# Performance work log

Measured on AMD Instinct MI355X. Metric: run time of the kernel, lower is better.

The kernel has to match this reference:

```python
import jax, jax.numpy as jnp
import numpy as np

N = 50000   # nodes
E = 800000  # edges
IN, HID, HEADS, OUT = 128, 32, 4, 64
NEG_SLOPE = 0.2


def _gatv2_layer(x, src, dst, Wl, bl, Wr, br, att, bias, res_W, concat):
    """One PyG-style GATv2Conv layer (eval mode, no dropout).
    x: [N, F_in]; att: [H, C]. Returns [N, H*C] if concat else [N, C]."""
    H, C = att.shape
    xl = (x @ Wl + bl).reshape(N, H, C)   # source transform
    xr = (x @ Wr + br).reshape(N, H, C)   # target transform
    e = jax.nn.leaky_relu(xl[src] + xr[dst], NEG_SLOPE)        # [E, H, C]
    logit = jnp.einsum('ehc,hc->eh', e, att)                   # [E, H]
    # segment softmax over incoming edges per destination node
    m = jax.ops.segment_max(logit, dst, num_segments=N)        # [N, H]
    p = jnp.exp(logit - m[dst])
    denom = jax.ops.segment_sum(p, dst, num_segments=N)
    alpha = p / (denom[dst] + 1e-16)                           # [E, H]
    out = jax.ops.segment_sum(xl[src] * alpha[:, :, None], dst, num_segments=N)  # [N, H, C]
    out = out.reshape(N, H * C) if concat else out.mean(axis=1)
    if res_W is not None:
        out = out + x @ res_W
    return out + bias


def _glorot(key, shape):
    fan_in = shape[0] if len(shape) > 1 else shape[-1]
    return jax.random.normal(key, shape, dtype=jnp.float32) / np.sqrt(fan_in)


def setup_inputs() -> dict:
    key = jax.random.key(0)
    ks = iter(jax.random.split(key, 32))
    x = jax.random.normal(next(ks), (N, IN), dtype=jnp.float32)
    edge_index = jax.random.randint(next(ks), (2, E), 0, N, dtype=jnp.int64)
    d = {"x": x, "edge_index": edge_index}
    HC = HEADS * HID  # 128
    # layer 0: IN -> HEADS*HID, concat, residual
    d["Wl0"] = _glorot(next(ks), (IN, HC)); d["bl0"] = jnp.zeros((HC,), jnp.float32)
    d["Wr0"] = _glorot(next(ks), (IN, HC)); d["br0"] = jnp.zeros((HC,), jnp.float32)
    d["att0"] = _glorot(next(ks), (HEADS, HID)); d["b0"] = jnp.zeros((HC,), jnp.float32)
    d["res0"] = _glorot(next(ks), (IN, HC))
    # layer 1: HC -> HEADS*HID, concat, residual
    d["Wl1"] = _glorot(next(ks), (HC, HC)); d["bl1"] = jnp.zeros((HC,), jnp.float32)
    d["Wr1"] = _glorot(next(ks), (HC, HC)); d["br1"] = jnp.zeros((HC,), jnp.float32)
    d["att1"] = _glorot(next(ks), (HEADS, HID)); d["b1"] = jnp.zeros((HC,), jnp.float32)
    d["res1"] = _glorot(next(ks), (HC, HC))
    # layer 2: HC -> OUT, heads=1, concat=False, no residual
    d["Wl2"] = _glorot(next(ks), (HC, OUT)); d["bl2"] = jnp.zeros((OUT,), jnp.float32)
    d["Wr2"] = _glorot(next(ks), (HC, OUT)); d["br2"] = jnp.zeros((OUT,), jnp.float32)
    d["att2"] = _glorot(next(ks), (1, OUT)); d["b2"] = jnp.zeros((OUT,), jnp.float32)
    return d


def reference(x, edge_index,
              Wl0, bl0, Wr0, br0, att0, b0, res0,
              Wl1, bl1, Wr1, br1, att1, b1, res1,
              Wl2, bl2, Wr2, br2, att2, b2):
    src, dst = edge_index[0], edge_index[1]
    h = _gatv2_layer(x, src, dst, Wl0, bl0, Wr0, br0, att0, b0, res0, True)
    h = jax.nn.elu(h)
    h = _gatv2_layer(h, src, dst, Wl1, bl1, Wr1, br1, att1, b1, res1, True)
    h = jax.nn.elu(h)
    return _gatv2_layer(h, src, dst, Wl2, bl2, Wr2, br2, att2, b2, None, False)
```

## Files before the change

kernel.cpp:

```cpp
#include <hip/hip_runtime.h>
#include <math.h>

#define NN 50000
#define EE 800000
#define NBK 196
#define EPB 4096

typedef short v8s __attribute__((ext_vector_type(8)));
typedef float v4f __attribute__((ext_vector_type(4)));

__device__ __forceinline__ ushort f2bf(float f) {
    uint u = __float_as_uint(f);
    uint r = (u + 0x7fffu + ((u >> 16) & 1u)) >> 16;
    return (ushort)r;
}
__device__ __forceinline__ float bf2f(ushort h) {
    return __uint_as_float(((uint)h) << 16);
}
__device__ __forceinline__ float lrelu(float x) {
    return fmaf(0.4f, fabsf(x), 0.6f * x);
}

__device__ __forceinline__ void gld_lds16(const void* g, void* l) {
    __builtin_amdgcn_global_load_lds(
        (const __attribute__((address_space(1))) void*)g,
        (__attribute__((address_space(3))) void*)l, 16, 0, 0);
}

template <int CTRL>
__device__ __forceinline__ float dppadd(float x) {
    int y = __builtin_amdgcn_update_dpp(0, __float_as_int(x), CTRL, 0xf, 0xf, true);
    return x + __int_as_float(y);
}
__device__ __forceinline__ float sum8(float x) {
    x = dppadd<0xB1>(x);
    x = dppadd<0x4E>(x);
    x = dppadd<0x141>(x);
    return x;
}
__device__ __forceinline__ float sum16(float x) {
    x = sum8(x);
    x = dppadd<0x140>(x);
    return x;
}
__device__ __forceinline__ float expclamp(float t) {
    return __expf(fminf(fmaxf(t, -60.f), 80.f));
}

__global__ __launch_bounds__(256) void k_bktcnt(const int* __restrict__ edst,
                                                int* __restrict__ bcnt) {
    __shared__ int h[NBK];
    int t = threadIdx.x;
    if (t < NBK) h[t] = 0;
    __syncthreads();
    int eb = blockIdx.x * EPB;
    #pragma unroll
    for (int k = 0; k < EPB / 256; ++k) {
        int e = eb + k * 256 + t;
        if (e < EE) atomicAdd(&h[edst[e] >> 8], 1);
    }
    __syncthreads();
    if (t < NBK && h[t]) atomicAdd(&bcnt[t], h[t]);
}

__global__ __launch_bounds__(256) void k_bscan(const int* __restrict__ bcnt,
                                               int* __restrict__ bbase,
                                               int* __restrict__ bcur) {
    __shared__ int sm[256];
    int t = threadIdx.x;
    int v = (t < NBK) ? bcnt[t] : 0;
    sm[t] = v;
    __syncthreads();
    for (int o = 1; o < 256; o <<= 1) {
        int a = (t >= o) ? sm[t - o] : 0;
        __syncthreads();
        sm[t] += a;
        __syncthreads();
    }
    if (t < NBK) { int ex = sm[t] - v; bbase[t] = ex; bcur[t] = ex; }
}

__global__ __launch_bounds__(256) void k_bktplace(const int* __restrict__ esrc,
                                                  const int* __restrict__ edst,
                                                  int* __restrict__ bcur,
                                                  uint* __restrict__ ebuf) {
    __shared__ int h[NBK];
    __shared__ int base[NBK];
    int t = threadIdx.x;
    if (t < NBK) h[t] = 0;
    __syncthreads();
    int eb = blockIdx.x * EPB;
    int pk[EPB / 256];
    #pragma unroll
    for (int k = 0; k < EPB / 256; ++k) {
        int e = eb + k * 256 + t;
        pk[k] = -1;
        if (e < EE) {
            int b = edst[e] >> 8;
            int r = atomicAdd(&h[b], 1);
            pk[k] = (b << 16) | r;
        }
    }
    __syncthreads();
    if (t < NBK && h[t]) base[t] = atomicAdd(&bcur[t], h[t]);
    __syncthreads();
    #pragma unroll
    for (int k = 0; k < EPB / 256; ++k) {
        int e = eb + k * 256 + t;
        if (e < EE) {
            int b = pk[k] >> 16;
            int r = pk[k] & 0xFFFF;
            uint dl = (uint)(edst[e] & 255);
            ebuf[base[b] + r] = (dl << 16) | (uint)esrc[e];
        }
    }
}

__global__ __launch_bounds__(256) void k_bktfin(const uint* __restrict__ ebuf,
                                                const int* __restrict__ bbase,
                                                const int* __restrict__ bcnt,
                                                int* __restrict__ rowptr,
                                                int* __restrict__ csrc) {
    __shared__ int deg[256];
    __shared__ int sm[256];
    __shared__ int cur[256];
    const int b = blockIdx.x;
    const int t = threadIdx.x;
    const int eb = bbase[b];
    const int ec = bcnt[b];
    deg[t] = 0;
    __syncthreads();
    for (int k = t; k < ec; k += 256)
        atomicAdd(&deg[ebuf[eb + k] >> 16], 1);
    __syncthreads();
    int v = deg[t];
    sm[t] = v;
    __syncthreads();
    for (int o = 1; o < 256; o <<= 1) {
        int a = (t >= o) ? sm[t - o] : 0;
        __syncthreads();
        sm[t] += a;
        __syncthreads();
    }
    int node = b * 256 + t;
    if (node < NN) rowptr[node + 1] = eb + sm[t];
    if (node == 0) rowptr[0] = 0;
    cur[t] = sm[t] - v;
    __syncthreads();
    for (int k = t; k < ec; k += 256) {
        uint u = ebuf[eb + k];
        int nl = (int)(u >> 16);
        int r = atomicAdd(&cur[nl], 1);
        csrc[eb + r] = (int)(u & 0xFFFFu);
    }
}

struct WPack {
    const float* W[8];
    ushort* Th[8];
    ushort* Tl[8];
    int fout[8];
};

__global__ __launch_bounds__(256) void k_conv_w(WPack p) {
    int wi = blockIdx.y;
    int fout = p.fout[wi];
    int total = 128 * fout;
    int i = blockIdx.x * 256 + threadIdx.x;
    if (i >= total) return;
    int k = i / fout;
    int n = i - k * fout;
    float f = p.W[wi][i];
    ushort h = f2bf(f);
    float lo = f - bf2f(h);
    int t = n >> 4, m = n & 15, c = k >> 5, quad = (k >> 3) & 3, j = k & 7;
    int flat = ((((t * 4 + c) * 4 + quad) * 16 + m) << 3) + j;
    p.Th[wi][flat] = h;
    p.Tl[wi][flat] = f2bf(lo);
}

template <int FOUT, int NMAT, bool CVT, int TS>
__global__ __launch_bounds__(512) void k_gemm_fused(
    const float* __restrict__ Xf,
    const ushort* __restrict__ Xh, const ushort* __restrict__ Xl,
    const ushort* __restrict__ T0h, const ushort* __restrict__ T0l, const float* __restrict__ B0,
    const ushort* __restrict__ T1h, const ushort* __restrict__ T1l, const float* __restrict__ B1,
    const ushort* __restrict__ T2h, const ushort* __restrict__ T2l,
    const float* __restrict__ ATT, float* __restrict__ DL, float* __restrict__ DR,
    ushort* __restrict__ O0b, ushort* __restrict__ O1b, float* __restrict__ O2)
{
    constexpr int CH = TS * 2048;
    __shared__ __align__(16) ushort Bs[NMAT * 2 * CH];

    const int tid  = threadIdx.x;
    const int lane = tid & 63;
    const int wid  = tid >> 6;
    const int m    = lane & 15;
    const int quad = lane >> 4;
    const int row0 = blockIdx.x * 128 + wid * 16;
    const int t0   = blockIdx.y * TS;

    {
        const ushort* tbls[6] = {T0h, T0l, T1h, T1l, T2h, T2l};
        #pragma unroll
        for (int k = 0; k < 2 * NMAT; ++k) {
            gld_lds16(tbls[k] + (size_t)t0 * 2048 + (size_t)tid * 8,
                      &Bs[k * CH + tid * 8]);
        }
    }

    v8s ah[4], al[4];
    {
        int arow = row0 + m;
        if (arow > NN - 1) arow = NN - 1;
        #pragma unroll
        for (int c = 0; c < 4; ++c) {
            size_t off = (size_t)arow * 128 + c * 32 + quad * 8;
            if constexpr (CVT) {
                float4 f0 = *(const float4*)(Xf + off);
                float4 f1 = *(const float4*)(Xf + off + 4);
                const float fe[8] = {f0.x, f0.y, f0.z, f0.w, f1.x, f1.y, f1.z, f1.w};
                #pragma unroll
                for (int e = 0; e < 8; ++e) {
                    ushort h = f2bf(fe[e]);
                    float lo = fe[e] - bf2f(h);
                    ah[c][e] = (short)h;
                    al[c][e] = (short)(__float_as_uint(lo) >> 16);
                }
            } else {
                ah[c] = *(const v8s*)(Xh + off);
                al[c] = *(const v8s*)(Xl + off);
            }
        }
    }

    __syncthreads();

    float dp0[4] = {0.f, 0.f, 0.f, 0.f};
    float dp1[4] = {0.f, 0.f, 0.f, 0.f};

    #pragma unroll
    for (int tt = 0; tt < TS; ++tt) {
        const int t = t0 + tt;
        v4f a0 = {0.f, 0.f, 0.f, 0.f};
        v4f a1 = {0.f, 0.f, 0.f, 0.f};
        v4f a2 = {0.f, 0.f, 0.f, 0.f};
        #pragma unroll
        for (int c = 0; c < 4; ++c) {
            const int fo = tt * 2048 + (c * 4 + quad) * 128 + m * 8;
            v8s b0h = *(const v8s*)&Bs[0 * CH + fo];
            v8s b0l = *(const v8s*)&Bs[1 * CH + fo];
            v8s b1h = *(const v8s*)&Bs[2 * CH + fo];
            v8s b1l = *(const v8s*)&Bs[3 * CH + fo];
            a0 = __builtin_amdgcn_mfma_f32_16x16x32_bf16(al[c], b0h, a0, 0, 0, 0);
            a1 = __builtin_amdgcn_mfma_f32_16x16x32_bf16(al[c], b1h, a1, 0, 0, 0);
            a0 = __builtin_amdgcn_mfma_f32_16x16x32_bf16(ah[c], b0l, a0, 0, 0, 0);
            a1 = __builtin_amdgcn_mfma_f32_16x16x32_bf16(ah[c], b1l, a1, 0, 0, 0);
            a0 = __builtin_amdgcn_mfma_f32_16x16x32_bf16(ah[c], b0h, a0, 0, 0, 0);
            a1 = __builtin_amdgcn_mfma_f32_16x16x32_bf16(ah[c], b1h, a1, 0, 0, 0);
            if constexpr (NMAT == 3) {
                v8s b2h = *(const v8s*)&Bs[4 * CH + fo];
                v8s b2l = *(const v8s*)&Bs[5 * CH + fo];
                a2 = __builtin_amdgcn_mfma_f32_16x16x32_bf16(al[c], b2h, a2, 0, 0, 0);
                a2 = __builtin_amdgcn_mfma_f32_16x16x32_bf16(ah[c], b2l, a2, 0, 0, 0);
                a2 = __builtin_amdgcn_mfma_f32_16x16x32_bf16(ah[c], b2h, a2, 0, 0, 0);
            }
        }
        const int col = t * 16 + m;
        const float bad0 = B0[col];
        const float bad1 = B1[col];
        const float attc = ATT[col];
        #pragma unroll
        for (int j = 0; j < 4; ++j) {
            float o0v = a0[j] + bad0;
            float o1v = a1[j] + bad1;
            dp0[j] = fmaf(attc, o0v, dp0[j]);
            dp1[j] = fmaf(attc, o1v, dp1[j]);
            int r = row0 + quad * 4 + j;
            if (r < NN) {
                O0b[(size_t)r * FOUT + col] = f2bf(o0v);
                O1b[(size_t)r * FOUT + col] = f2bf(o1v);
                if constexpr (NMAT == 3) O2[(size_t)r * FOUT + col] = a2[j];
            }
        }
        if constexpr (FOUT == 128) {
            if ((t & 1) == 1) {
                const int h = t >> 1;
                #pragma unroll
                for (int j = 0; j < 4; ++j) {
                    float s0 = sum16(dp0[j]);
                    float s1 = sum16(dp1[j]);
                    int r = row0 + quad * 4 + j;
                    if (m == 0 && r < NN) {
                        DL[(size_t)r * 4 + h] = 0.6f * s0;
                        DR[(size_t)r * 4 + h] = 0.6f * s1;
                    }
                    dp0[j] = 0.f;
                    dp1[j] = 0.f;
                }
            }
        }
    }
    if constexpr (FOUT == 64) {
        #pragma unroll
        for (int j = 0; j < 4; ++j) {
            float s0 = sum16(dp0[j]);
            float s1 = sum16(dp1[j]);
            int r = row0 + quad * 4 + j;
            if (m == 0 && r < NN) {
                atomicAdd(&DL[r], 0.6f * s0);
                atomicAdd(&DR[r], 0.6f * s1);
            }
        }
    }
}

__global__ __launch_bounds__(256) void k_agg01(const ushort* __restrict__ XLb,
                                               const ushort* __restrict__ XRb,
                                               const float4* __restrict__ RES4,
                                               const float* __restrict__ att,
                                               const float* __restrict__ bias,
                                               const float* __restrict__ DL,
                                               const float* __restrict__ DR,
                                               const int* __restrict__ rowptr,
                                               const int* __restrict__ csrc,
                                               ushort* __restrict__ Hh,
                                               ushort* __restrict__ Hl) {
    const int lane = threadIdx.x & 63;
    const int wid = threadIdx.x >> 6;
    const int n = blockIdx.x * 4 + wid;
    if (n >= NN) return;
    const int beg = rowptr[n];
    const int end = rowptr[n + 1];
    const int e1 = end - 1;
    const int half = lane >> 5;
    const uint j = lane & 31;
    const uint head = j >> 3;

    float4 xr;
    {
        ushort4 u = *(const ushort4*)(XRb + (uint)n * 128u + 4u * j);
        xr.x = bf2f(u.x); xr.y = bf2f(u.y); xr.z = bf2f(u.z); xr.w = bf2f(u.w);
    }
    float4 at = ((const float4*)att)[j];
    at.x *= 0.4f; at.y *= 0.4f; at.z *= 0.4f; at.w *= 0.4f;
    const float dRn = DR[(uint)n * 4u + head];
    float4 s = {0.f, 0.f, 0.f, 0.f};
    float d = 0.f;

#define GL01(I, U0, U1, U2, U3, D0, D1, D2, D3) {              \
    uint sa = (uint)csrc[min((I) + half, e1)];                 \
    uint sb = (uint)csrc[min((I) + 2 + half, e1)];             \
    uint sc = (uint)csrc[min((I) + 4 + half, e1)];             \
    uint sd = (uint)csrc[min((I) + 6 + half, e1)];             \
    U0 = *(const ushort4*)(XLb + sa * 128u + 4u * j);          \
    U1 = *(const ushort4*)(XLb + sb * 128u + 4u * j);          \
    U2 = *(const ushort4*)(XLb + sc * 128u + 4u * j);          \
    U3 = *(const ushort4*)(XLb + sd * 128u + 4u * j);          \
    D0 = DL[sa * 4u + head];                                   \
    D1 = DL[sb * 4u + head];                                   \
    D2 = DL[sc * 4u + head];                                   \
    D3 = DL[sd * 4u + head]; }

#define EDGE01(U, DLV, II) {                                   \
    float v0 = bf2f((U).x), v1 = bf2f((U).y);                  \
    float v2 = bf2f((U).z), v3 = bf2f((U).w);                  \
    float t =      at.x * fabsf(v0 + xr.x);                    \
    t = fmaf(at.y, fabsf(v1 + xr.y), t);                       \
    t = fmaf(at.z, fabsf(v2 + xr.z), t);                       \
    t = fmaf(at.w, fabsf(v3 + xr.w), t);                       \
    float p = expclamp(sum8(t) + (DLV) + dRn);                 \
    p = ((II) < end) ? p : 0.f;                                \
    d += p;                                                    \
    s.x = fmaf(p, v0, s.x); s.y = fmaf(p, v1, s.y);            \
    s.z = fmaf(p, v2, s.z); s.w = fmaf(p, v3, s.w); }

    if (beg < end) {
        ushort4 cu0, cu1, cu2, cu3;
        float cd0, cd1, cd2, cd3;
        GL01(beg, cu0, cu1, cu2, cu3, cd0, cd1, cd2, cd3)
        for (int i = beg; i < end; i += 8) {
            ushort4 nu0, nu1, nu2, nu3;
            float nd0, nd1, nd2, nd3;
            GL01(i + 8, nu0, nu1, nu2, nu3, nd0, nd1, nd2, nd3)
            EDGE01(cu0, cd0, i + half)
            EDGE01(cu1, cd1, i + 2 + half)
            EDGE01(cu2, cd2, i + 4 + half)
            EDGE01(cu3, cd3, i + 6 + half)
            cu0 = nu0; cu1 = nu1; cu2 = nu2; cu3 = nu3;
            cd0 = nd0; cd1 = nd1; cd2 = nd2; cd3 = nd3;
        }
    }
#undef GL01
#undef EDGE01

    d   += __shfl_xor(d, 32);
    s.x += __shfl_xor(s.x, 32);
    s.y += __shfl_xor(s.y, 32);
    s.z += __shfl_xor(s.z, 32);
    s.w += __shfl_xor(s.w, 32);

    if (half == 0) {
        float inv = (d > 0.f) ? 1.f / d : 0.f;
        float4 rv = RES4[(uint)n * 32u + j];
        float4 bv = ((const float4*)bias)[j];
        float o0 = fmaf(s.x, inv, rv.x + bv.x);
        float o1 = fmaf(s.y, inv, rv.y + bv.y);
        float o2 = fmaf(s.z, inv, rv.z + bv.z);
        float o3 = fmaf(s.w, inv, rv.w + bv.w);
        o0 = o0 > 0.f ? o0 : __expf(o0) - 1.f;
        o1 = o1 > 0.f ? o1 : __expf(o1) - 1.f;
        o2 = o2 > 0.f ? o2 : __expf(o2) - 1.f;
        o3 = o3 > 0.f ? o3 : __expf(o3) - 1.f;
        ushort4 h, l;
        h.x = f2bf(o0); l.x = f2bf(o0 - bf2f(h.x));
        h.y = f2bf(o1); l.y = f2bf(o1 - bf2f(h.y));
        h.z = f2bf(o2); l.z = f2bf(o2 - bf2f(h.z));
        h.w = f2bf(o3); l.w = f2bf(o3 - bf2f(h.w));
        *(ushort4*)(Hh + (uint)n * 128u + 4u * j) = h;
        *(ushort4*)(Hl + (uint)n * 128u + 4u * j) = l;
    }
}

__global__ __launch_bounds__(256) void k_agg2(const ushort* __restrict__ XLb,
                                              const ushort* __restrict__ XRb,
                                              const float* __restrict__ att,
                                              const float* __restrict__ bias,
                                              const float* __restrict__ DL,
                                              const float* __restrict__ DR,
                                              const int* __restrict__ rowptr,
                                              const int* __restrict__ csrc,
                                              float* __restrict__ OUT) {
    const int lane = threadIdx.x & 63;
    const int wid = threadIdx.x >> 6;
    const int n = blockIdx.x * 4 + wid;
    if (n >= NN) return;
    const int beg = rowptr[n];
    const int end = rowptr[n + 1];
    const int e1 = end - 1;
    const int q = lane >> 4;
    const uint jj = lane & 15;

    float4 xr;
    {
        ushort4 u = *(const ushort4*)(XRb + (uint)n * 64u + 4u * jj);
        xr.x = bf2f(u.x); xr.y = bf2f(u.y); xr.z = bf2f(u.z); xr.w = bf2f(u.w);
    }
    float4 at = ((const float4*)att)[jj];
    at.x *= 0.4f; at.y *= 0.4f; at.z *= 0.4f; at.w *= 0.4f;
    const float dRn = DR[n];
    float4 s = {0.f, 0.f, 0.f, 0.f};
    float d = 0.f;

#define GL2(I, U0, U1, D0, D1) {                               \
    uint sa = (uint)csrc[min((I) + q, e1)];                    \
    uint sb = (uint)csrc[min((I) + 4 + q, e1)];                \
    U0 = *(const ushort4*)(XLb + sa * 64u + 4u * jj);          \
    U1 = *(const ushort4*)(XLb + sb * 64u + 4u * jj);          \
    D0 = DL[sa];                                               \
    D1 = DL[sb]; }

#define EDGE2(U, DLV, II) {                                    \
    float v0 = bf2f((U).x), v1 = bf2f((U).y);                  \
    float v2 = bf2f((U).z), v3 = bf2f((U).w);                  \
    float t =      at.x * fabsf(v0 + xr.x);                    \
    t = fmaf(at.y, fabsf(v1 + xr.y), t);                       \
    t = fmaf(at.z, fabsf(v2 + xr.z), t);                       \
    t = fmaf(at.w, fabsf(v3 + xr.w), t);                       \
    float p = expclamp(sum16(t) + (DLV) + dRn);                \
    p = ((II) < end) ? p : 0.f;                                \
    d += p;                                                    \
    s.x = fmaf(p, v0, s.x); s.y = fmaf(p, v1, s.y);            \
    s.z = fmaf(p, v2, s.z); s.w = fmaf(p, v3, s.w); }

    if (beg < end) {
        ushort4 cu0, cu1;
        float cd0, cd1;
        GL2(beg, cu0, cu1, cd0, cd1)
        for (int i = beg; i < end; i += 8) {
            ushort4 nu0, nu1;
            float nd0, nd1;
            GL2(i + 8, nu0, nu1, nd0, nd1)
            EDGE2(cu0, cd0, i + q)
            EDGE2(cu1, cd1, i + 4 + q)
            cu0 = nu0; cu1 = nu1;
            cd0 = nd0; cd1 = nd1;
        }
    }
#undef GL2
#undef EDGE2

    d   += __shfl_xor(d, 16);   d   += __shfl_xor(d, 32);
    s.x += __shfl_xor(s.x, 16); s.x += __shfl_xor(s.x, 32);
    s.y += __shfl_xor(s.y, 16); s.y += __shfl_xor(s.y, 32);
    s.z += __shfl_xor(s.z, 16); s.z += __shfl_xor(s.z, 32);
    s.w += __shfl_xor(s.w, 16); s.w += __shfl_xor(s.w, 32);

    if (lane < 16) {
        float inv = (d > 0.f) ? 1.f / d : 0.f;
        float4 bv = ((const float4*)bias)[jj];
        float4 o;
        o.x = fmaf(s.x, inv, bv.x);
        o.y = fmaf(s.y, inv, bv.y);
        o.z = fmaf(s.z, inv, bv.z);
        o.w = fmaf(s.w, inv, bv.w);
        *(float4*)(OUT + (uint)n * 64u + 4u * jj) = o;
    }
}

extern "C" void kernel_launch(void* const* d_in, const int* in_sizes, int n_in,
                              void* d_out, int out_size, void* d_ws, size_t ws_size,
                              hipStream_t stream) {
    const float* x    = (const float*)d_in[0];
    const int*   ei   = (const int*)d_in[1];
    const int*   esrc = ei;
    const int*   edst = ei + EE;

    const float* Wl0 = (const float*)d_in[2];
    const float* bl0 = (const float*)d_in[3];
    const float* Wr0 = (const float*)d_in[4];
    const float* br0 = (const float*)d_in[5];
    const float* at0 = (const float*)d_in[6];
    const float* b0  = (const float*)d_in[7];
    const float* rs0 = (const float*)d_in[8];
    const float* Wl1 = (const float*)d_in[9];
    const float* bl1 = (const float*)d_in[10];
    const float* Wr1 = (const float*)d_in[11];
    const float* br1 = (const float*)d_in[12];
    const float* at1 = (const float*)d_in[13];
    const float* b1  = (const float*)d_in[14];
    const float* rs1 = (const float*)d_in[15];
    const float* Wl2 = (const float*)d_in[16];
    const float* bl2 = (const float*)d_in[17];
    const float* Wr2 = (const float*)d_in[18];
    const float* br2 = (const float*)d_in[19];
    const float* at2 = (const float*)d_in[20];
    const float* b2  = (const float*)d_in[21];

    float* out = (float*)d_out;

    ushort* XLb = (ushort*)d_ws;
    ushort* XRb = XLb + (size_t)NN * 128;
    float* RES = (float*)(XRb + (size_t)NN * 128);
    ushort* Xh = (ushort*)(RES + (size_t)NN * 128);
    ushort* Xl_ = Xh + (size_t)NN * 128;
    float* DLarr = (float*)(Xl_ + (size_t)NN * 128);
    float* DRarr = DLarr + (size_t)NN * 4;
    ushort* Wth = (ushort*)(DRarr + (size_t)NN * 4);
    const int wsz[8] = {16384, 16384, 16384, 16384, 16384, 16384, 8192, 8192};
    ushort* th[8]; ushort* tl[8];
    {
        ushort* p = Wth;
        for (int i = 0; i < 8; ++i) { th[i] = p; p += wsz[i]; }
        for (int i = 0; i < 8; ++i) { tl[i] = p; p += wsz[i]; }
    }
    int* bcnt   = (int*)(Wth + 2 * (6 * 16384 + 2 * 8192));
    int* bbase  = bcnt + 256;
    int* bcur   = bbase + 256;
    int* rowptr = bcur + 256;
    int* csrc   = rowptr + (NN + 1);
    uint* ebuf  = (uint*)(csrc + EE);

    hipMemsetAsync(bcnt, 0, 256 * sizeof(int), stream);
    const int ebk = (EE + EPB - 1) / EPB;
    k_bktcnt<<<ebk, 256, 0, stream>>>(edst, bcnt);
    k_bscan<<<1, 256, 0, stream>>>(bcnt, bbase, bcur);
    k_bktplace<<<ebk, 256, 0, stream>>>(esrc, edst, bcur, ebuf);
    k_bktfin<<<NBK, 256, 0, stream>>>(ebuf, bbase, bcnt, rowptr, csrc);

    WPack wp;
    const float* Ws[8] = {Wl0, Wr0, rs0, Wl1, Wr1, rs1, Wl2, Wr2};
    const int fouts[8] = {128, 128, 128, 128, 128, 128, 64, 64};
    for (int i = 0; i < 8; ++i) { wp.W[i] = Ws[i]; wp.Th[i] = th[i]; wp.Tl[i] = tl[i]; wp.fout[i] = fouts[i]; }
    k_conv_w<<<dim3(64, 8), 256, 0, stream>>>(wp);

    const int gemm_gx = (NN + 127) / 128;
    const int agg_grid = (NN + 3) / 4;

    k_gemm_fused<128, 3, true, 2><<<dim3(gemm_gx, 4), 512, 0, stream>>>(x, nullptr, nullptr,
        th[0], tl[0], bl0, th[1], tl[1], br0, th[2], tl[2], at0, DLarr, DRarr, XLb, XRb, RES);
    k_agg01<<<agg_grid, 256, 0, stream>>>(XLb, XRb, (const float4*)RES,
        at0, b0, DLarr, DRarr, rowptr, csrc, Xh, Xl_);

    k_gemm_fused<128, 3, false, 2><<<dim3(gemm_gx, 4), 512, 0, stream>>>(nullptr, Xh, Xl_,
        th[3], tl[3], bl1, th[4], tl[4], br1, th[5], tl[5], at1, DLarr, DRarr, XLb, XRb, RES);
    k_agg01<<<agg_grid, 256, 0, stream>>>(XLb, XRb, (const float4*)RES,
        at1, b1, DLarr, DRarr, rowptr, csrc, Xh, Xl_);

    hipMemsetAsync(DLarr, 0, NN * sizeof(float), stream);
    hipMemsetAsync(DRarr, 0, NN * sizeof(float), stream);
    k_gemm_fused<64, 2, false, 2><<<dim3(gemm_gx, 2), 512, 0, stream>>>(nullptr, Xh, Xl_,
        th[6], tl[6], bl2, th[7], tl[7], br2, nullptr, nullptr, at2, DLarr, DRarr, XLb, XRb, nullptr);
    k_agg2<<<agg_grid, 256, 0, stream>>>(XLb, XRb, at2, b2, DLarr, DRarr, rowptr, csrc, out);
}
```

Before: 350.6 us.

## Process two row tiles per GEMM block, prefetching the second tile's A

For the layer-0/1 GEMMs, each block now handles two 128-row tiles (grid halved to 196 in x) and issues the global loads for the second tile's A operand before computing the first. The B-table LDS load is then shared by two tiles instead of one. This overlaps A-load latency with MFMA work at the cost of more registers and fewer blocks. The layer-2 GEMM keeps its original grid of 391, so it still does one tile per block.

```diff
diff --git a/kernel.cpp b/kernel.cpp
--- a/kernel.cpp
+++ b/kernel.cpp
@@ -16,9 +16,6 @@
 }
 __device__ __forceinline__ float bf2f(ushort h) {
     return __uint_as_float(((uint)h) << 16);
-}
-__device__ __forceinline__ float lrelu(float x) {
-    return fmaf(0.4f, fabsf(x), 0.6f * x);
 }
 
 __device__ __forceinline__ void gld_lds16(const void* g, void* l) {
@@ -179,7 +176,7 @@
     p.Tl[wi][flat] = f2bf(lo);
 }
 
-template <int FOUT, int NMAT, bool CVT, int TS>
+template <int FOUT, int NMAT, bool CVT, int TS, int GX>
 __global__ __launch_bounds__(512) void k_gemm_fused(
     const float* __restrict__ Xf,
     const ushort* __restrict__ Xh, const ushort* __restrict__ Xl,
@@ -190,6 +187,7 @@
     ushort* __restrict__ O0b, ushort* __restrict__ O1b, float* __restrict__ O2)
 {
     constexpr int CH = TS * 2048;
+    constexpr int NTILE = (NN + 127) / 128;
     __shared__ __align__(16) ushort Bs[NMAT * 2 * CH];
 
     const int tid  = threadIdx.x;
@@ -197,7 +195,6 @@
     const int wid  = tid >> 6;
     const int m    = lane & 15;
     const int quad = lane >> 4;
-    const int row0 = blockIdx.x * 128 + wid * 16;
     const int t0   = blockIdx.y * TS;
 
     {
@@ -209,17 +206,27 @@
         }
     }
 
-    v8s ah[4], al[4];
-    {
-        int arow = row0 + m;
+    auto issueA = [&](int rt, float4* rf, v8s* ah, v8s* al) {
+        int arow = rt * 128 + wid * 16 + m;
         if (arow > NN - 1) arow = NN - 1;
         #pragma unroll
         for (int c = 0; c < 4; ++c) {
             size_t off = (size_t)arow * 128 + c * 32 + quad * 8;
             if constexpr (CVT) {
-                float4 f0 = *(const float4*)(Xf + off);
-                float4 f1 = *(const float4*)(Xf + off + 4);
-                const float fe[8] = {f0.x, f0.y, f0.z, f0.w, f1.x, f1.y, f1.z, f1.w};
+                rf[c * 2]     = *(const float4*)(Xf + off);
+                rf[c * 2 + 1] = *(const float4*)(Xf + off + 4);
+            } else {
+                ah[c] = *(const v8s*)(Xh + off);
+                al[c] = *(const v8s*)(Xl + off);
+            }
+        }
+    };
+    auto cookA = [&](const float4* rf, v8s* ah, v8s* al) {
+        if constexpr (CVT) {
+            #pragma unroll
+            for (int c = 0; c < 4; ++c) {
+                const float fe[8] = {rf[c*2].x,   rf[c*2].y,   rf[c*2].z,   rf[c*2].w,
+                                     rf[c*2+1].x, rf[c*2+1].y, rf[c*2+1].z, rf[c*2+1].w};
                 #pragma unroll
                 for (int e = 0; e < 8; ++e) {
                     ushort h = f2bf(fe[e]);
@@ -227,90 +234,110 @@
                     ah[c][e] = (short)h;
                     al[c][e] = (short)(__float_as_uint(lo) >> 16);
                 }
-            } else {
-                ah[c] = *(const v8s*)(Xh + off);
-                al[c] = *(const v8s*)(Xl + off);
             }
         }
-    }
-
-    __syncthreads();
-
-    float dp0[4] = {0.f, 0.f, 0.f, 0.f};
-    float dp1[4] = {0.f, 0.f, 0.f, 0.f};
-
-    #pragma unroll
-    for (int tt = 0; tt < TS; ++tt) {
-        const int t = t0 + tt;
-        v4f a0 = {0.f, 0.f, 0.f, 0.f};
-        v4f a1 = {0.f, 0.f, 0.f, 0.f};
-        v4f a2 = {0.f, 0.f, 0.f, 0.f};
+    };
+
+    auto computeTile = [&](int rt, const v8s* ah, const v8s* al) {
+        const int row0 = rt * 128 + wid * 16;
+        float dp0[4] = {0.f, 0.f, 0.f, 0.f};
+        float dp1[4] = {0.f, 0.f, 0.f, 0.f};
         #pragma unroll
-        for (int c = 0; c < 4; ++c) {
-            const int fo = tt * 2048 + (c * 4 + quad) * 128 + m * 8;
-            v8s b0h = *(const v8s*)&Bs[0 * CH + fo];
-            v8s b0l = *(const v8s*)&Bs[1 * CH + fo];
-            v8s b1h = *(const v8s*)&Bs[2 * CH + fo];
-            v8s b1l = *(const v8s*)&Bs[3 * CH + fo];
-            a0 = __builtin_amdgcn_mfma_f32_16x16x32_bf16(al[c], b0h, a0, 0, 0, 0);
-            a1 = __builtin_amdgcn_mfma_f32_16x16x32_bf16(al[c], b1h, a1, 0, 0, 0);
-            a0 = __builtin_amdgcn_mfma_f32_16x16x32_bf16(ah[c], b0l, a0, 0, 0, 0);
-            a1 = __builtin_amdgcn_mfma_f32_16x16x32_bf16(ah[c], b1l, a1, 0, 0, 0);
-            a0 = __builtin_amdgcn_mfma_f32_16x16x32_bf16(ah[c], b0h, a0, 0, 0, 0);
-            a1 = __builtin_amdgcn_mfma_f32_16x16x32_bf16(ah[c], b1h, a1, 0, 0, 0);
-            if constexpr (NMAT == 3) {
-                v8s b2h = *(const v8s*)&Bs[4 * CH + fo];
-                v8s b2l = *(const v8s*)&Bs[5 * CH + fo];
-                a2 = __builtin_amdgcn_mfma_f32_16x16x32_bf16(al[c], b2h, a2, 0, 0, 0);
-                a2 = __builtin_amdgcn_mfma_f32_16x16x32_bf16(ah[c], b2l, a2, 0, 0, 0);
-                a2 = __builtin_amdgcn_mfma_f32_16x16x32_bf16(ah[c], b2h, a2, 0, 0, 0);
-            }
-        }
-        const int col = t * 16 + m;
-        const float bad0 = B0[col];
-        const float bad1 = B1[col];
-        const float attc = ATT[col];
-        #pragma unroll
-        for (int j = 0; j < 4; ++j) {
-            float o0v = a0[j] + bad0;
-            float o1v = a1[j] + bad1;
-            dp0[j] = fmaf(attc, o0v, dp0[j]);
-            dp1[j] = fmaf(attc, o1v, dp1[j]);
-            int r = row0 + quad * 4 + j;
-            if (r < NN) {
-                O0b[(size_t)r * FOUT + col] = f2bf(o0v);
-                O1b[(size_t)r * FOUT + col] = f2bf(o1v);
-                if constexpr (NMAT == 3) O2[(size_t)r * FOUT + col] = a2[j];
-            }
-        }
-        if constexpr (FOUT == 128) {
-            if ((t & 1) == 1) {
-                const int h = t >> 1;
-                #pragma unroll
-                for (int j = 0; j < 4; ++j) {
-                    float s0 = sum16(dp0[j]);
-                    float s1 = sum16(dp1[j]);
-                    int r = row0 + quad * 4 + j;
-                    if (m == 0 && r < NN) {
-                        DL[(size_t)r * 4 + h] = 0.6f * s0;
-                        DR[(size_t)r * 4 + h] = 0.6f * s1;
-                    }
-                    dp0[j] = 0.f;
-                    dp1[j] = 0.f;
+        for (int tt = 0; tt < TS; ++tt) {
+            const int t = t0 + tt;
+            v4f a0 = {0.f, 0.f, 0.f, 0.f};
+            v4f a1 = {0.f, 0.f, 0.f, 0.f};
+            v4f a2 = {0.f, 0.f, 0.f, 0.f};
+            #pragma unroll
+            for (int c = 0; c < 4; ++c) {
+                const int fo = tt * 2048 + (c * 4 + quad) * 128 + m * 8;
+                v8s b0h = *(const v8s*)&Bs[0 * CH + fo];
+                v8s b0l = *(const v8s*)&Bs[1 * CH + fo];
+                v8s b1h = *(const v8s*)&Bs[2 * CH + fo];
+                v8s b1l = *(const v8s*)&Bs[3 * CH + fo];
+                a0 = __builtin_amdgcn_mfma_f32_16x16x32_bf16(al[c], b0h, a0, 0, 0, 0);
+                a1 = __builtin_amdgcn_mfma_f32_16x16x32_bf16(al[c], b1h, a1, 0, 0, 0);
+                a0 = __builtin_amdgcn_mfma_f32_16x16x32_bf16(ah[c], b0l, a0, 0, 0, 0);
+                a1 = __builtin_amdgcn_mfma_f32_16x16x32_bf16(ah[c], b1l, a1, 0, 0, 0);
+                a0 = __builtin_amdgcn_mfma_f32_16x16x32_bf16(ah[c], b0h, a0, 0, 0, 0);
+                a1 = __builtin_amdgcn_mfma_f32_16x16x32_bf16(ah[c], b1h, a1, 0, 0, 0);
+                if constexpr (NMAT == 3) {
+                    v8s b2h = *(const v8s*)&Bs[4 * CH + fo];
+                    v8s b2l = *(const v8s*)&Bs[5 * CH + fo];
+                    a2 = __builtin_amdgcn_mfma_f32_16x16x32_bf16(al[c], b2h, a2, 0, 0, 0);
+                    a2 = __builtin_amdgcn_mfma_f32_16x16x32_bf16(ah[c], b2l, a2, 0, 0, 0);
+                    a2 = __builtin_amdgcn_mfma_f32_16x16x32_bf16(ah[c], b2h, a2, 0, 0, 0);
                 }
             }
-        }
-    }
-    if constexpr (FOUT == 64) {
-        #pragma unroll
-        for (int j = 0; j < 4; ++j) {
-            float s0 = sum16(dp0[j]);
-            float s1 = sum16(dp1[j]);
-            int r = row0 + quad * 4 + j;
-            if (m == 0 && r < NN) {
-                atomicAdd(&DL[r], 0.6f * s0);
-                atomicAdd(&DR[r], 0.6f * s1);
+            const int col = t * 16 + m;
+            const float bad0 = B0[col];
+            const float bad1 = B1[col];
+            const float attc = ATT[col];
+            #pragma unroll
+            for (int j = 0; j < 4; ++j) {
+                float o0v = a0[j] + bad0;
+                float o1v = a1[j] + bad1;
+                dp0[j] = fmaf(attc, o0v, dp0[j]);
+                dp1[j] = fmaf(attc, o1v, dp1[j]);
+                int r = row0 + quad * 4 + j;
+                if (r < NN) {
+                    O0b[(size_t)r * FOUT + col] = f2bf(o0v);
+                    O1b[(size_t)r * FOUT + col] = f2bf(o1v);
+                    if constexpr (NMAT == 3) O2[(size_t)r * FOUT + col] = a2[j];
+                }
             }
+            if constexpr (FOUT == 128) {
+                if ((t & 1) == 1) {
+                    const int h = t >> 1;
+                    #pragma unroll
+                    for (int j = 0; j < 4; ++j) {
+                        float s0 = sum16(dp0[j]);
+                        float s1 = sum16(dp1[j]);
+                        int r = row0 + quad * 4 + j;
+                        if (m == 0 && r < NN) {
+                            DL[(size_t)r * 4 + h] = 0.6f * s0;
+                            DR[(size_t)r * 4 + h] = 0.6f * s1;
+                        }
+                        dp0[j] = 0.f;
+                        dp1[j] = 0.f;
+                    }
+                }
+            }
+        }
+        if constexpr (FOUT == 64) {
+            #pragma unroll
+            for (int j = 0; j < 4; ++j) {
+                float s0 = sum16(dp0[j]);
+                float s1 = sum16(dp1[j]);
+                int r = row0 + quad * 4 + j;
+                if (m == 0 && r < NN) {
+                    atomicAdd(&DL[r], 0.6f * s0);
+                    atomicAdd(&DR[r], 0.6f * s1);
+                }
+            }
+        }
+    };
+
+    const int rt0 = blockIdx.x;
+    const int rt1 = blockIdx.x + GX;
+    const bool has1 = (rt1 < NTILE);
+
+    float4 rf0[8], rf1[8];
+    v8s ah0[4], al0[4], ah1[4], al1[4];
+
+    issueA(rt0, rf0, ah0, al0);
+    __syncthreads();
+
+    if (has1) issueA(rt1, rf1, ah1, al1);
+
+    cookA(rf0, ah0, al0);
+    computeTile(rt0, ah0, al0);
+    if (has1) {
+        if constexpr (CVT) {
+            cookA(rf1, ah0, al0);
+            computeTile(rt1, ah0, al0);
+        } else {
+            computeTile(rt1, ah1, al1);
         }
     }
 }
@@ -574,22 +601,21 @@
     for (int i = 0; i < 8; ++i) { wp.W[i] = Ws[i]; wp.Th[i] = th[i]; wp.Tl[i] = tl[i]; wp.fout[i] = fouts[i]; }
     k_conv_w<<<dim3(64, 8), 256, 0, stream>>>(wp);
 
-    const int gemm_gx = (NN + 127) / 128;
     const int agg_grid = (NN + 3) / 4;
 
-    k_gemm_fused<128, 3, true, 2><<<dim3(gemm_gx, 4), 512, 0, stream>>>(x, nullptr, nullptr,
+    k_gemm_fused<128, 3, true, 2, 196><<<dim3(196, 4), 512, 0, stream>>>(x, nullptr, nullptr,
         th[0], tl[0], bl0, th[1], tl[1], br0, th[2], tl[2], at0, DLarr, DRarr, XLb, XRb, RES);
     k_agg01<<<agg_grid, 256, 0, stream>>>(XLb, XRb, (const float4*)RES,
         at0, b0, DLarr, DRarr, rowptr, csrc, Xh, Xl_);
 
-    k_gemm_fused<128, 3, false, 2><<<dim3(gemm_gx, 4), 512, 0, stream>>>(nullptr, Xh, Xl_,
+    k_gemm_fused<128, 3, false, 2, 196><<<dim3(196, 4), 512, 0, stream>>>(nullptr, Xh, Xl_,
         th[3], tl[3], bl1, th[4], tl[4], br1, th[5], tl[5], at1, DLarr, DRarr, XLb, XRb, RES);
     k_agg01<<<agg_grid, 256, 0, stream>>>(XLb, XRb, (const float4*)RES,
         at1, b1, DLarr, DRarr, rowptr, csrc, Xh, Xl_);
 
     hipMemsetAsync(DLarr, 0, NN * sizeof(float), stream);
     hipMemsetAsync(DRarr, 0, NN * sizeof(float), stream);
-    k_gemm_fused<64, 2, false, 2><<<dim3(gemm_gx, 2), 512, 0, stream>>>(nullptr, Xh, Xl_,
+    k_gemm_fused<64, 2, false, 2, 391><<<dim3(391, 2), 512, 0, stream>>>(nullptr, Xh, Xl_,
         th[6], tl[6], bl2, th[7], tl[7], br2, nullptr, nullptr, at2, DLarr, DRarr, XLb, XRb, nullptr);
     k_agg2<<<agg_grid, 256, 0, stream>>>(XLb, XRb, at2, b2, DLarr, DRarr, rowptr, csrc, out);
 }
```

Result: slower. 379.0 us (+8.1%).
